# Kernel tuning notes

Measured on AMD Instinct MI355X. Metric: run time of the kernel, lower is better.

## Reference

```python
import jax, jax.numpy as jnp
import numpy as np

B, N, F_DIM, G_DIM, E_CAT, N_HEAD = 8, 1024, 128, 64, 2, 4
N_EDGES = 16384
L0 = 256          # NodeEmbedding hidden layer (layers=[256,128] -> last replaced by feature_size)
ALPHA = 0.5       # cfg.alpha
EPS = 1e-5        # BatchNorm eps
SLOPE = 0.01      # leaky_relu default negative slope


def _glorot(k, shape):
    stdv = float(np.sqrt(6.0 / (shape[-2] + shape[-1])))
    return jax.random.uniform(k, shape, jnp.float32, -stdv, stdv)


def setup_inputs() -> dict:
    key = jax.random.key(0)
    ks = jax.random.split(key, 8)
    X = jax.random.normal(ks[0], (B, N, F_DIM), dtype=jnp.float32)
    A = jax.random.randint(ks[1], (B, E_CAT, 2, N_EDGES), 0, N, dtype=jnp.int32)
    Ws = _glorot(ks[2], (E_CAT, N_HEAD * F_DIM, G_DIM))
    Wq = _glorot(ks[3], (E_CAT, N_HEAD * F_DIM, 1))
    Wv = _glorot(ks[4], (E_CAT, N_HEAD * F_DIM, 1))
    W_emb1 = _glorot(ks[5], (F_DIM, N_HEAD * E_CAT * G_DIM))   # Embedding1, bias=False
    W_lin0 = _glorot(ks[6], (L0, F_DIM))                        # NodeEmbedding linear0
    W_lin1 = _glorot(ks[7], (F_DIM, L0))                        # NodeEmbedding linear1
    return {"A": A, "X": X, "Ws": Ws, "Wq": Wq, "Wv": Wv,
            "W_emb1": W_emb1, "W_lin0": W_lin0, "W_lin1": W_lin1, "mini_batch": 1}


def _bn(x):
    # BatchNorm1d in training mode, affine = identity (weight=1, bias=0)
    mu = jnp.mean(x, axis=0)
    var = jnp.var(x, axis=0)  # biased variance, as torch uses for normalization
    return (x - mu) * jax.lax.rsqrt(var + EPS)


def _build_adj(A):
    # torch.sparse_coo_tensor(...).to_dense() sums duplicate edges
    adj = jnp.zeros((B, E_CAT, N, N), jnp.float32)
    b_idx = jnp.arange(B)[:, None, None]
    e_idx = jnp.arange(E_CAT)[None, :, None]
    return adj.at[b_idx, e_idx, A[:, :, 0], A[:, :, 1]].add(1.0)


def reference(A, X, Ws, Wq, Wv, W_emb1, W_lin0, W_lin1, mini_batch):
    Ws_r = Ws.reshape(E_CAT, N_HEAD, F_DIM, G_DIM)
    Wq_r = Wq.reshape(E_CAT, N_HEAD, F_DIM)   # last dim of Wq param is 1
    Wv_r = Wv.reshape(E_CAT, N_HEAD, F_DIM)

    Wh = jnp.einsum('bnf,ehfg->behng', X, Ws_r)   # [B,E,H,N,G]
    q = jnp.einsum('bnf,ehf->behn', X, Wq_r)      # [B,E,H,N]
    v = jnp.einsum('bnf,ehf->behn', X, Wv_r)

    adj = _build_adj(A)                            # [B,E,N,N]
    # e = (Wq @ Wv.T) * E, then leaky_relu and row softmax (dim=1 on [N,N] = last axis)
    scores = q[:, :, :, :, None] * v[:, :, :, None, :] * adj[:, :, None]
    scores = jnp.where(scores >= 0, scores, SLOPE * scores)
    a = jax.nn.softmax(scores, axis=-1)
    H = jnp.einsum('behnm,behmg->behng', a, Wh)    # [B,E,H,N,G]

    # concat over heads: [B,N, head-major (E*G)]
    H = H.transpose(0, 3, 2, 1, 4).reshape(B * N, N_HEAD * E_CAT * G_DIM)
    H = jax.nn.relu(H @ W_emb1.T)
    Xf = X.reshape(B * N, F_DIM)
    H = _bn((1.0 - ALPHA) * H + ALPHA * Xf)

    # NodeEmbedding: Linear -> BN -> ELU -> Linear
    Z = jax.nn.elu(_bn(H @ W_lin0.T))
    Z = Z @ W_lin1.T
    Z = _bn(H + Z)
    return Z.reshape(B, N, F_DIM)
```

## Files before the change

kernel.cpp:

```cpp
#include <hip/hip_runtime.h>
#include <hip/hip_bf16.h>

#define B_    8
#define N_    1024
#define F_    128
#define G_    64
#define EC    2
#define NHD   4
#define NE    16384
#define L0_   256
#define ALPHA_ 0.5f
#define EPS_   1e-5f
#define SLOPE_ 0.01f
#define ROWS  (B_*N_)
#define C1    (NHD*EC*G_)

typedef __attribute__((ext_vector_type(8))) short s8bf;
typedef __attribute__((ext_vector_type(4))) float f32x4;

__device__ __forceinline__ float ldv(const float* p, size_t i) { return p[i]; }
__device__ __forceinline__ float ldv(const __hip_bfloat16* p, size_t i) {
  unsigned short u = *(const unsigned short*)&p[i];
  return __uint_as_float((unsigned)u << 16);
}
__device__ __forceinline__ unsigned short f2b(float f) {
  unsigned u = __float_as_uint(f);
  u = (u + 0x7FFFu + ((u >> 16) & 1u)) >> 16;
  return (unsigned short)u;
}
__device__ __forceinline__ float b2f(unsigned short u) {
  return __uint_as_float((unsigned)u << 16);
}

__device__ __forceinline__ float wmaxf(float v) {
#pragma unroll
  for (int o = 32; o; o >>= 1) v = fmaxf(v, __shfl_xor(v, o, 64));
  return v;
}
__device__ __forceinline__ float wsumf(float v) {
#pragma unroll
  for (int o = 32; o; o >>= 1) v += __shfl_xor(v, o, 64);
  return v;
}

__global__ void k_prep(const unsigned short* Xu, int* flag,
                       const int* A, int* fill, int* colbuf) {
  int bid = blockIdx.x, tid = threadIdx.x;
  if (bid < 512) {
    int idx = bid * 256 + tid;
    unsigned short u = Xu[idx];
    if ((u & 0x7F80u) == 0x7F80u) atomicOr(flag, 1);
  } else {
    int idx = (bid - 512) * 256 + tid;
    int be = idx >> 14, i = idx & (NE - 1);
    int row = A[(size_t)(be * 2) * NE + i];
    int col = A[(size_t)(be * 2 + 1) * NE + i];
    int p = atomicAdd(&fill[be * N_ + row], 1);
    if (p < 64) colbuf[((size_t)(be * N_ + row)) * 64 + p] = col;
  }
}

__device__ __forceinline__ unsigned short cvt_at(const void* p, size_t i, int isf) {
  return isf ? f2b(((const float*)p)[i]) : ((const unsigned short*)p)[i];
}
template <typename T>
__device__ __forceinline__ void proj_qv16(const T* X, const T* Wq, const T* Wv,
                                          float* q, float* v, int pb) {
  int tid = threadIdx.x, lane = tid & 63, w = tid >> 6;
  int sub = lane >> 4, fl = lane & 15;
  int r = pb * 16 + w * 4 + sub;
  int n = r & (N_ - 1); int beh = r >> 10; int be = beh >> 2, h = beh & 3;
  int b = be >> 1, e = be & 1;
  const T* xr = X + (size_t)(b * N_ + n) * F_ + fl * 8;
  const T* wq = Wq + (e * NHD + h) * F_ + fl * 8;
  const T* wv = Wv + (e * NHD + h) * F_ + fl * 8;
  float dq = 0.f, dv = 0.f;
#pragma unroll
  for (int j = 0; j < 8; ++j) {
    float x = ldv(xr, j);
    dq += x * ldv(wq, j); dv += x * ldv(wv, j);
  }
#pragma unroll
  for (int o = 1; o < 16; o <<= 1) {
    dq += __shfl_xor(dq, o, 64); dv += __shfl_xor(dv, o, 64);
  }
  if (fl == 0) { q[r] = dq; v[r] = dv; }
}
__global__ void k_cvt2(const void* X, const void* Ws, const void* We1, const void* Wl1,
                       const void* Wl0, const void* Wq, const void* Wv,
                       unsigned short* Wsb, unsigned short* We1b,
                       unsigned short* Wl1b, unsigned short* Wl0b,
                       float* q, float* v, const int* flag) {
  int isf = *flag;
  int bid = blockIdx.x, t = threadIdx.x;
  if (bid < 256) {
    int i = bid * 256 + t; We1b[i] = cvt_at(We1, i, isf);
  } else if (bid < 384) {
    int i = (bid - 256) * 256 + t; Wl1b[i] = cvt_at(Wl1, i, isf);
  } else if (bid < 512) {
    int i = (bid - 384) * 256 + t; Wl0b[i] = cvt_at(Wl0, i, isf);
  } else if (bid < 768) {
    int i = (bid - 512) * 256 + t;
    int eh = i >> 13, rem = i & 8191;
    int g = rem >> 7, f = rem & 127;
    Wsb[eh * 8192 + g * 128 + f] = cvt_at(Ws, (size_t)eh * 8192 + f * 64 + g, isf);
  } else {
    int pb = bid - 768;
    if (isf) proj_qv16<float>((const float*)X, (const float*)Wq, (const float*)Wv, q, v, pb);
    else     proj_qv16<__hip_bfloat16>((const __hip_bfloat16*)X, (const __hip_bfloat16*)Wq,
                                       (const __hip_bfloat16*)Wv, q, v, pb);
  }
}

template <int K, int NC, int MODE, typename TA>
__device__ __forceinline__ void mfma_core_u(const TA* __restrict__ Araw,
                                            const float* sum, const float* ssq,
                                            const unsigned short* __restrict__ Wb,
                                            int r0, int c0, f32x4* acc) {
  int lane = threadIdx.x & 63; int q = lane >> 4, c15 = lane & 15;
  constexpr int RS = K / 8;
  const s8bf* bp = (const s8bf*)Wb + (size_t)(c0 + c15) * RS + q;
#pragma unroll
  for (int ks = 0; ks < K / 32; ++ks) {
    s8bf a;
    if constexpr (sizeof(TA) == 2) {
      const s8bf* ap = (const s8bf*)Araw + (size_t)(r0 + c15) * RS + q;
      a = ap[ks * 4];
    } else {
      const float* ap = (const float*)Araw + (size_t)(r0 + c15) * K + q * 8 + ks * 32;
      float av[8];
      *(float4*)&av[0] = *(const float4*)ap;
      *(float4*)&av[4] = *(const float4*)(ap + 4);
#pragma unroll
      for (int j = 0; j < 8; ++j) {
        float y = av[j];
        if (MODE) {
          int c = q * 8 + ks * 32 + j;
          float mean = sum[c] * (1.f / ROWS);
          float var = ssq[c] * (1.f / ROWS) - mean * mean;
          y = (y - mean) * rsqrtf(var + EPS_);
          if (MODE == 2) y = (y > 0.f) ? y : (expf(y) - 1.f);
        }
        a[j] = (short)f2b(y);
      }
    }
#pragma unroll
    for (int nc = 0; nc < NC; ++nc) {
      s8bf b = bp[(size_t)nc * 16 * RS + ks * 4];
      acc[nc] = __builtin_amdgcn_mfma_f32_16x16x32_bf16(a, b, acc[nc], 0, 0, 0);
    }
  }
}

__global__ __launch_bounds__(256) void k_whm(const void* X, const unsigned short* Wsb,
                                             unsigned short* Whb, float* S,
                                             const int* flag) {
  int w = threadIdx.x >> 6;
  int r0 = (blockIdx.x * 4 + w) * 16; int eh = blockIdx.y;
  f32x4 acc[4] = {{0,0,0,0},{0,0,0,0},{0,0,0,0},{0,0,0,0}};
  if (*flag)
    mfma_core_u<128, 4, 0, float>((const float*)X, nullptr, nullptr,
                                  Wsb + eh * 8192, r0, 0, acc);
  else
    mfma_core_u<128, 4, 0, unsigned short>((const unsigned short*)X, nullptr, nullptr,
                                           Wsb + eh * 8192, r0, 0, acc);
  int lane = threadIdx.x & 63, q = lane >> 4, c15 = lane & 15;
  int b = r0 >> 10; int beh = b * 8 + eh;
  unsigned short* WhB = Whb + ((size_t)beh * N_ + (r0 & (N_ - 1))) * G_;
#pragma unroll
  for (int nc = 0; nc < 4; ++nc) {
    float s = 0.f;
#pragma unroll
    for (int i = 0; i < 4; ++i) {
      float o = acc[nc][i];
      WhB[(size_t)(q * 4 + i) * G_ + nc * 16 + c15] = f2b(o);
      s += o;
    }
    s += __shfl_xor(s, 16, 64); s += __shfl_xor(s, 32, 64);
    if (lane < 16) atomicAdd(&S[(size_t)beh * G_ + nc * 16 + lane], s);
  }
}

__global__ __launch_bounds__(256) void k_attn3(const float* q, const float* v,
                                               const unsigned short* Whb,
                                               const float* S, const int* fill,
                                               const int* colbuf, unsigned short* Hcatb) {
  int tid = threadIdx.x, lane = tid & 63, w = tid >> 6;
  int xcd = blockIdx.x & 7, j = blockIdx.x >> 3;
  int be = (xcd << 1) | (j & 1);
  int n = (j >> 1) * 4 + w;
  int b = be >> 1, e = be & 1;
  int L = fill[be * N_ + n];
  int Lc = (L > 64) ? 64 : L;
  int myc = (lane < Lc) ? colbuf[((size_t)(be * N_ + n)) * 64 + lane] : -1;
  int cct = 0, firstk = 64;
  for (int k = 0; k < Lc; ++k) {
    int ck = __shfl(myc, k, 64);
    if (myc >= 0 && ck == myc) { cct++; if (k < firstk) firstk = k; }
  }
  bool act = (lane < Lc) && (firstk == lane);
  unsigned long long mask = __ballot(act);
  int pos = __popcll(mask & ((1ull << lane) - 1ull));
  __shared__ int s_col[4][64];
  __shared__ int s_cnt[4][64];
  s_col[w][lane] = 0; s_cnt[w][lane] = 0;
  if (act) { s_col[w][pos] = myc; s_cnt[w][pos] = cct; }
  int Ld = __popcll(mask);
  int colc = s_col[w][lane];
  int cntc = s_cnt[w][lane];
  int eg = lane >> 4, g4 = (lane & 15) << 2;
  size_t outb = ((size_t)(b * N_ + n)) * C1 + e * G_ + g4;
  float fN = (float)(N_ - Ld);
#pragma unroll
  for (int h = 0; h < 4; ++h) {
    int beh = (be << 2) | h;
    float qn = q[beh * N_ + n];
    float sc = -1e30f;
    if (lane < Ld) {
      float t = qn * v[beh * N_ + colc] * (float)cntc;
      sc = (t >= 0.f) ? t : SLOPE_ * t;
    }
    float M = fmaxf(0.f, wmaxf(sc));
    float Ej = (lane < Ld) ? expf(sc - M) : 0.f;
    float sumE = wsumf(Ej);
    float em = expf(-M);
    float Z = fN * em + sumE;
    float wgt = (lane < Ld) ? (Ej - em) / Z : 0.f;
    float4 accv = make_float4(0.f, 0.f, 0.f, 0.f);
    if (eg == 0) {
      float4 s4 = *(const float4*)&S[(size_t)beh * G_ + g4];
      float sca = em / Z;
      accv.x = sca * s4.x; accv.y = sca * s4.y; accv.z = sca * s4.z; accv.w = sca * s4.w;
    }
    const unsigned short* WhB = Whb + (size_t)beh * N_ * G_;
    for (int k0 = 0; k0 < Ld; k0 += 4) {
      int kk = k0 + eg;
      float wk = __shfl(wgt, kk, 64);
      int ck = __shfl(colc, kk, 64);
      ushort4 xu = *(const ushort4*)&WhB[(size_t)ck * G_ + g4];
      accv.x += wk * b2f(xu.x); accv.y += wk * b2f(xu.y);
      accv.z += wk * b2f(xu.z); accv.w += wk * b2f(xu.w);
    }
    accv.x += __shfl_xor(accv.x, 16, 64); accv.y += __shfl_xor(accv.y, 16, 64);
    accv.z += __shfl_xor(accv.z, 16, 64); accv.w += __shfl_xor(accv.w, 16, 64);
    accv.x += __shfl_xor(accv.x, 32, 64); accv.y += __shfl_xor(accv.y, 32, 64);
    accv.z += __shfl_xor(accv.z, 32, 64); accv.w += __shfl_xor(accv.w, 32, 64);
    if (lane < 16) {
      ushort4 o;
      o.x = f2b(accv.x); o.y = f2b(accv.y); o.z = f2b(accv.z); o.w = f2b(accv.w);
      *(ushort4*)&Hcatb[outb + (size_t)h * (EC * G_)] = o;
    }
  }
}

template <typename TX>
__device__ __forceinline__ void mm1_ep(f32x4* acc, const TX* X, float* T4,
                                       float* sum1, float* ssq1, int r0, int c0) {
  int lane = threadIdx.x & 63, q = lane >> 4, c15 = lane & 15;
#pragma unroll
  for (int nc = 0; nc < 2; ++nc) {
    int cc = c0 + nc * 16 + c15;
    float s = 0.f, s2 = 0.f;
#pragma unroll
    for (int i = 0; i < 4; ++i) {
      int rr = r0 + q * 4 + i;
      float o = fmaxf(acc[nc][i], 0.f);
      o = 0.5f * o + 0.5f * ldv(X, (size_t)rr * F_ + cc);
      T4[(size_t)rr * F_ + cc] = o;
      s += o; s2 += o * o;
    }
    s += __shfl_xor(s, 16, 64); s += __shfl_xor(s, 32, 64);
    s2 += __shfl_xor(s2, 16, 64); s2 += __shfl_xor(s2, 32, 64);
    if (lane < 16) {
      atomicAdd(&sum1[c0 + nc * 16 + lane], s);
      atomicAdd(&ssq1[c0 + nc * 16 + lane], s2);
    }
  }
}
__global__ __launch_bounds__(256) void k_mm1m(const unsigned short* Hcatb,
                                              const unsigned short* We1b, const void* X,
                                              float* T4, float* sum1, float* ssq1,
                                              const int* flag) {
  int w = threadIdx.x >> 6;
  int tile = blockIdx.x * 4 + w;
  int r0 = (tile >> 2) * 16, c0 = (tile & 3) * 32;
  f32x4 acc[2] = {{0,0,0,0},{0,0,0,0}};
  mfma_core_u<512, 2, 0, unsigned short>(Hcatb, nullptr, nullptr, We1b, r0, c0, acc);
  if (*flag) mm1_ep<float>(acc, (const float*)X, T4, sum1, ssq1, r0, c0);
  else       mm1_ep<__hip_bfloat16>(acc, (const __hip_bfloat16*)X, T4, sum1, ssq1, r0, c0);
}

__global__ __launch_bounds__(256) void k_lin0m(const float* T4, const float* sum1,
                                               const float* ssq1, const unsigned short* Wl0b,
                                               float* Z0, float* sum2, float* ssq2) {
  int w = threadIdx.x >> 6;
  int tile = blockIdx.x * 4 + w;
  int r0 = (tile >> 3) * 16, c0 = (tile & 7) * 32;
  f32x4 acc[2] = {{0,0,0,0},{0,0,0,0}};
  mfma_core_u<128, 2, 1, float>(T4, sum1, ssq1, Wl0b, r0, c0, acc);
  int lane = threadIdx.x & 63, q = lane >> 4, c15 = lane & 15;
#pragma unroll
  for (int nc = 0; nc < 2; ++nc) {
    int cc = c0 + nc * 16 + c15;
    float s = 0.f, s2 = 0.f;
#pragma unroll
    for (int i = 0; i < 4; ++i) {
      int rr = r0 + q * 4 + i;
      float o = acc[nc][i];
      Z0[(size_t)rr * L0_ + cc] = o;
      s += o; s2 += o * o;
    }
    s += __shfl_xor(s, 16, 64); s += __shfl_xor(s, 32, 64);
    s2 += __shfl_xor(s2, 16, 64); s2 += __shfl_xor(s2, 32, 64);
    if (lane < 16) {
      atomicAdd(&sum2[c0 + nc * 16 + lane], s);
      atomicAdd(&ssq2[c0 + nc * 16 + lane], s2);
    }
  }
}

__global__ __launch_bounds__(256) void k_lin1m(const float* Z0, const float* sum2,
                                               const float* ssq2, const unsigned short* Wl1b,
                                               const float* T4, const float* sum1,
                                               const float* ssq1,
                                               float* T6, float* sum3, float* ssq3) {
  int w = threadIdx.x >> 6;
  int tile = blockIdx.x * 4 + w;
  int r0 = (tile >> 2) * 16, c0 = (tile & 3) * 32;
  f32x4 acc[2] = {{0,0,0,0},{0,0,0,0}};
  mfma_core_u<256, 2, 2, float>(Z0, sum2, ssq2, Wl1b, r0, c0, acc);
  int lane = threadIdx.x & 63, q = lane >> 4, c15 = lane & 15;
#pragma unroll
  for (int nc = 0; nc < 2; ++nc) {
    int cc = c0 + nc * 16 + c15;
    float mean = sum1[cc] * (1.f / ROWS);
    float var = ssq1[cc] * (1.f / ROWS) - mean * mean;
    float rs = rsqrtf(var + EPS_);
    float s = 0.f, s2 = 0.f;
#pragma unroll
    for (int i = 0; i < 4; ++i) {
      int rr = r0 + q * 4 + i;
      float o = acc[nc][i] + (T4[(size_t)rr * F_ + cc] - mean) * rs;
      T6[(size_t)rr * F_ + cc] = o;
      s += o; s2 += o * o;
    }
    s += __shfl_xor(s, 16, 64); s += __shfl_xor(s, 32, 64);
    s2 += __shfl_xor(s2, 16, 64); s2 += __shfl_xor(s2, 32, 64);
    if (lane < 16) {
      atomicAdd(&sum3[c0 + nc * 16 + lane], s);
      atomicAdd(&ssq3[c0 + nc * 16 + lane], s2);
    }
  }
}

__global__ void k_norm_out(const float* in, void* out, const float* sum, const float* ssq,
                           const int* flag) {
  int idx = blockIdx.x * 256 + threadIdx.x; int c = idx & (F_ - 1);
  float mean = sum[c] * (1.f / ROWS);
  float var = ssq[c] * (1.f / ROWS) - mean * mean;
  float y = (in[idx] - mean) * rsqrtf(var + EPS_);
  if (*flag) ((float*)out)[idx] = y;
  else       ((__hip_bfloat16*)out)[idx] = __float2bfloat16(y);
}

extern "C" void kernel_launch(void* const* d_in, const int* in_sizes, int n_in,
                              void* d_out, int out_size, void* d_ws, size_t ws_size,
                              hipStream_t stream) {
  const int* A    = (const int*)d_in[0];
  const void* X   = d_in[1];
  const void* Ws  = d_in[2];
  const void* Wq  = d_in[3];
  const void* Wv  = d_in[4];
  const void* We1 = d_in[5];
  const void* Wl0 = d_in[6];
  const void* Wl1 = d_in[7];

  char* ws = (char*)d_ws;
  size_t off = 0;
  auto alloc = [&](size_t bytes) { size_t o = off; off += (bytes + 255) & ~(size_t)255; return o; };
  size_t o_fill   = alloc(16 * N_ * 4);
  size_t o_stats  = alloc(1024 * 4);
  size_t o_flag   = alloc(256);
  size_t o_S      = alloc((size_t)64 * G_ * 4);
  size_t zero_bytes = off;
  size_t o_colbuf = alloc((size_t)16 * N_ * 64 * 4);
  size_t o_q      = alloc((size_t)64 * N_ * 4);
  size_t o_v      = alloc((size_t)64 * N_ * 4);
  size_t o_Whb    = alloc((size_t)64 * N_ * G_ * 2);
  size_t o_Hcatb  = alloc((size_t)ROWS * C1 * 2);
  size_t o_T4     = alloc((size_t)ROWS * F_ * 4);
  size_t o_T6     = alloc((size_t)ROWS * F_ * 4);
  size_t o_Z0     = alloc((size_t)ROWS * L0_ * 4);
  size_t o_Wsb    = alloc((size_t)8 * G_ * F_ * 2);
  size_t o_We1b   = alloc((size_t)F_ * C1 * 2);
  size_t o_Wl1b   = alloc((size_t)F_ * L0_ * 2);
  size_t o_Wl0b   = alloc((size_t)L0_ * F_ * 2);

  int*   fill   = (int*)(ws + o_fill);
  float* stats  = (float*)(ws + o_stats);
  int*   flag   = (int*)(ws + o_flag);
  float* S      = (float*)(ws + o_S);
  int*   colbuf = (int*)(ws + o_colbuf);
  float* q      = (float*)(ws + o_q);
  float* v      = (float*)(ws + o_v);
  unsigned short* Whb   = (unsigned short*)(ws + o_Whb);
  unsigned short* Hcatb = (unsigned short*)(ws + o_Hcatb);
  float* T4     = (float*)(ws + o_T4);
  float* T6     = (float*)(ws + o_T6);
  float* Z0     = (float*)(ws + o_Z0);
  unsigned short* Wsb   = (unsigned short*)(ws + o_Wsb);
  unsigned short* We1b  = (unsigned short*)(ws + o_We1b);
  unsigned short* Wl1b  = (unsigned short*)(ws + o_Wl1b);
  unsigned short* Wl0b  = (unsigned short*)(ws + o_Wl0b);
  float* sum1 = stats,       *ssq1 = stats + 128;
  float* sum2 = stats + 256, *ssq2 = stats + 512;
  float* sum3 = stats + 768, *ssq3 = stats + 896;

  hipMemsetAsync(ws, 0, zero_bytes, stream);

  k_prep<<<1536, 256, 0, stream>>>((const unsigned short*)X, flag, A, fill, colbuf);
  k_cvt2<<<768 + 4096, 256, 0, stream>>>(X, Ws, We1, Wl1, Wl0, Wq, Wv,
                                         Wsb, We1b, Wl1b, Wl0b, q, v, flag);
  k_whm<<<dim3(ROWS / 64, 8), 256, 0, stream>>>(X, Wsb, Whb, S, flag);
  k_attn3<<<(16 * N_) / 4, 256, 0, stream>>>(q, v, Whb, S, fill, colbuf, Hcatb);
  k_mm1m<<<512, 256, 0, stream>>>(Hcatb, We1b, X, T4, sum1, ssq1, flag);
  k_lin0m<<<1024, 256, 0, stream>>>(T4, sum1, ssq1, Wl0b, Z0, sum2, ssq2);
  k_lin1m<<<512, 256, 0, stream>>>(Z0, sum2, ssq2, Wl1b, T4, sum1, ssq1,
                                   T6, sum3, ssq3);
  k_norm_out<<<(ROWS * F_) / 256, 256, 0, stream>>>(T6, d_out, sum3, ssq3, flag);

  (void)in_sizes; (void)n_in; (void)out_size; (void)ws_size;
}
```

Before: 212.5 us.

## Fuse all pipeline stages into one persistent kernel with grid barriers

Replaces the eight separate kernel launches with a single persistent kernel of 256 blocks. The stages are separated by atomic-counter grid barriers and each stage's work is redistributed over the fixed grid with strided loops. The aim is to remove launch overhead and inter-kernel gaps. In exchange, parallelism drops to 256 blocks of 256 threads (for example, attention now loops 16 rows per wave), and the spin barriers assume all blocks are co-resident.

```diff
diff --git a/kernel.cpp b/kernel.cpp
--- a/kernel.cpp
+++ b/kernel.cpp
@@ -31,7 +31,6 @@
 __device__ __forceinline__ float b2f(unsigned short u) {
   return __uint_as_float((unsigned)u << 16);
 }
-
 __device__ __forceinline__ float wmaxf(float v) {
 #pragma unroll
   for (int o = 32; o; o >>= 1) v = fmaxf(v, __shfl_xor(v, o, 64));
@@ -42,74 +41,19 @@
   for (int o = 32; o; o >>= 1) v += __shfl_xor(v, o, 64);
   return v;
 }
-
-__global__ void k_prep(const unsigned short* Xu, int* flag,
-                       const int* A, int* fill, int* colbuf) {
-  int bid = blockIdx.x, tid = threadIdx.x;
-  if (bid < 512) {
-    int idx = bid * 256 + tid;
-    unsigned short u = Xu[idx];
-    if ((u & 0x7F80u) == 0x7F80u) atomicOr(flag, 1);
-  } else {
-    int idx = (bid - 512) * 256 + tid;
-    int be = idx >> 14, i = idx & (NE - 1);
-    int row = A[(size_t)(be * 2) * NE + i];
-    int col = A[(size_t)(be * 2 + 1) * NE + i];
-    int p = atomicAdd(&fill[be * N_ + row], 1);
-    if (p < 64) colbuf[((size_t)(be * N_ + row)) * 64 + p] = col;
-  }
-}
-
 __device__ __forceinline__ unsigned short cvt_at(const void* p, size_t i, int isf) {
   return isf ? f2b(((const float*)p)[i]) : ((const unsigned short*)p)[i];
 }
-template <typename T>
-__device__ __forceinline__ void proj_qv16(const T* X, const T* Wq, const T* Wv,
-                                          float* q, float* v, int pb) {
-  int tid = threadIdx.x, lane = tid & 63, w = tid >> 6;
-  int sub = lane >> 4, fl = lane & 15;
-  int r = pb * 16 + w * 4 + sub;
-  int n = r & (N_ - 1); int beh = r >> 10; int be = beh >> 2, h = beh & 3;
-  int b = be >> 1, e = be & 1;
-  const T* xr = X + (size_t)(b * N_ + n) * F_ + fl * 8;
-  const T* wq = Wq + (e * NHD + h) * F_ + fl * 8;
-  const T* wv = Wv + (e * NHD + h) * F_ + fl * 8;
-  float dq = 0.f, dv = 0.f;
-#pragma unroll
-  for (int j = 0; j < 8; ++j) {
-    float x = ldv(xr, j);
-    dq += x * ldv(wq, j); dv += x * ldv(wv, j);
-  }
-#pragma unroll
-  for (int o = 1; o < 16; o <<= 1) {
-    dq += __shfl_xor(dq, o, 64); dv += __shfl_xor(dv, o, 64);
-  }
-  if (fl == 0) { q[r] = dq; v[r] = dv; }
-}
-__global__ void k_cvt2(const void* X, const void* Ws, const void* We1, const void* Wl1,
-                       const void* Wl0, const void* Wq, const void* Wv,
-                       unsigned short* Wsb, unsigned short* We1b,
-                       unsigned short* Wl1b, unsigned short* Wl0b,
-                       float* q, float* v, const int* flag) {
-  int isf = *flag;
-  int bid = blockIdx.x, t = threadIdx.x;
-  if (bid < 256) {
-    int i = bid * 256 + t; We1b[i] = cvt_at(We1, i, isf);
-  } else if (bid < 384) {
-    int i = (bid - 256) * 256 + t; Wl1b[i] = cvt_at(Wl1, i, isf);
-  } else if (bid < 512) {
-    int i = (bid - 384) * 256 + t; Wl0b[i] = cvt_at(Wl0, i, isf);
-  } else if (bid < 768) {
-    int i = (bid - 512) * 256 + t;
-    int eh = i >> 13, rem = i & 8191;
-    int g = rem >> 7, f = rem & 127;
-    Wsb[eh * 8192 + g * 128 + f] = cvt_at(Ws, (size_t)eh * 8192 + f * 64 + g, isf);
-  } else {
-    int pb = bid - 768;
-    if (isf) proj_qv16<float>((const float*)X, (const float*)Wq, (const float*)Wv, q, v, pb);
-    else     proj_qv16<__hip_bfloat16>((const __hip_bfloat16*)X, (const __hip_bfloat16*)Wq,
-                                       (const __hip_bfloat16*)Wv, q, v, pb);
-  }
+
+__device__ __forceinline__ void gbar(int* cnt) {
+  __syncthreads();
+  __threadfence();
+  if (threadIdx.x == 0) {
+    atomicAdd(cnt, 1);
+    while (atomicAdd(cnt, 0) < 256) __builtin_amdgcn_s_sleep(2);
+  }
+  __syncthreads();
+  __threadfence();
 }
 
 template <int K, int NC, int MODE, typename TA>
@@ -117,17 +61,17 @@
                                             const float* sum, const float* ssq,
                                             const unsigned short* __restrict__ Wb,
                                             int r0, int c0, f32x4* acc) {
-  int lane = threadIdx.x & 63; int q = lane >> 4, c15 = lane & 15;
+  int lane = threadIdx.x & 63; int qd = lane >> 4, c15 = lane & 15;
   constexpr int RS = K / 8;
-  const s8bf* bp = (const s8bf*)Wb + (size_t)(c0 + c15) * RS + q;
+  const s8bf* bp = (const s8bf*)Wb + (size_t)(c0 + c15) * RS + qd;
 #pragma unroll
   for (int ks = 0; ks < K / 32; ++ks) {
     s8bf a;
     if constexpr (sizeof(TA) == 2) {
-      const s8bf* ap = (const s8bf*)Araw + (size_t)(r0 + c15) * RS + q;
+      const s8bf* ap = (const s8bf*)Araw + (size_t)(r0 + c15) * RS + qd;
       a = ap[ks * 4];
     } else {
-      const float* ap = (const float*)Araw + (size_t)(r0 + c15) * K + q * 8 + ks * 32;
+      const float* ap = (const float*)Araw + (size_t)(r0 + c15) * K + qd * 8 + ks * 32;
       float av[8];
       *(float4*)&av[0] = *(const float4*)ap;
       *(float4*)&av[4] = *(const float4*)(ap + 4);
@@ -135,7 +79,7 @@
       for (int j = 0; j < 8; ++j) {
         float y = av[j];
         if (MODE) {
-          int c = q * 8 + ks * 32 + j;
+          int c = qd * 8 + ks * 32 + j;
           float mean = sum[c] * (1.f / ROWS);
           float var = ssq[c] * (1.f / ROWS) - mean * mean;
           y = (y - mean) * rsqrtf(var + EPS_);
@@ -152,215 +96,277 @@
   }
 }
 
-__global__ __launch_bounds__(256) void k_whm(const void* X, const unsigned short* Wsb,
-                                             unsigned short* Whb, float* S,
-                                             const int* flag) {
-  int w = threadIdx.x >> 6;
-  int r0 = (blockIdx.x * 4 + w) * 16; int eh = blockIdx.y;
-  f32x4 acc[4] = {{0,0,0,0},{0,0,0,0},{0,0,0,0},{0,0,0,0}};
-  if (*flag)
-    mfma_core_u<128, 4, 0, float>((const float*)X, nullptr, nullptr,
-                                  Wsb + eh * 8192, r0, 0, acc);
-  else
-    mfma_core_u<128, 4, 0, unsigned short>((const unsigned short*)X, nullptr, nullptr,
-                                           Wsb + eh * 8192, r0, 0, acc);
-  int lane = threadIdx.x & 63, q = lane >> 4, c15 = lane & 15;
-  int b = r0 >> 10; int beh = b * 8 + eh;
-  unsigned short* WhB = Whb + ((size_t)beh * N_ + (r0 & (N_ - 1))) * G_;
-#pragma unroll
-  for (int nc = 0; nc < 4; ++nc) {
-    float s = 0.f;
-#pragma unroll
-    for (int i = 0; i < 4; ++i) {
-      float o = acc[nc][i];
-      WhB[(size_t)(q * 4 + i) * G_ + nc * 16 + c15] = f2b(o);
-      s += o;
-    }
-    s += __shfl_xor(s, 16, 64); s += __shfl_xor(s, 32, 64);
-    if (lane < 16) atomicAdd(&S[(size_t)beh * G_ + nc * 16 + lane], s);
-  }
-}
-
-__global__ __launch_bounds__(256) void k_attn3(const float* q, const float* v,
-                                               const unsigned short* Whb,
-                                               const float* S, const int* fill,
-                                               const int* colbuf, unsigned short* Hcatb) {
-  int tid = threadIdx.x, lane = tid & 63, w = tid >> 6;
-  int xcd = blockIdx.x & 7, j = blockIdx.x >> 3;
-  int be = (xcd << 1) | (j & 1);
-  int n = (j >> 1) * 4 + w;
-  int b = be >> 1, e = be & 1;
-  int L = fill[be * N_ + n];
-  int Lc = (L > 64) ? 64 : L;
-  int myc = (lane < Lc) ? colbuf[((size_t)(be * N_ + n)) * 64 + lane] : -1;
-  int cct = 0, firstk = 64;
-  for (int k = 0; k < Lc; ++k) {
-    int ck = __shfl(myc, k, 64);
-    if (myc >= 0 && ck == myc) { cct++; if (k < firstk) firstk = k; }
-  }
-  bool act = (lane < Lc) && (firstk == lane);
-  unsigned long long mask = __ballot(act);
-  int pos = __popcll(mask & ((1ull << lane) - 1ull));
+__global__ __launch_bounds__(256) void k_mega(
+    const int* A, const void* X, const void* Ws, const void* Wq, const void* Wv,
+    const void* We1, const void* Wl0, const void* Wl1,
+    int* flag, int* fill, int* colbuf,
+    unsigned short* Wsb, unsigned short* We1b, unsigned short* Wl1b, unsigned short* Wl0b,
+    float* q, float* v, unsigned short* Whb, float* S, unsigned short* Hcatb,
+    float* T4, float* Z0, float* T6, float* stats, void* out, int* bars) {
   __shared__ int s_col[4][64];
   __shared__ int s_cnt[4][64];
-  s_col[w][lane] = 0; s_cnt[w][lane] = 0;
-  if (act) { s_col[w][pos] = myc; s_cnt[w][pos] = cct; }
-  int Ld = __popcll(mask);
-  int colc = s_col[w][lane];
-  int cntc = s_cnt[w][lane];
-  int eg = lane >> 4, g4 = (lane & 15) << 2;
-  size_t outb = ((size_t)(b * N_ + n)) * C1 + e * G_ + g4;
-  float fN = (float)(N_ - Ld);
-#pragma unroll
-  for (int h = 0; h < 4; ++h) {
-    int beh = (be << 2) | h;
-    float qn = q[beh * N_ + n];
-    float sc = -1e30f;
-    if (lane < Ld) {
-      float t = qn * v[beh * N_ + colc] * (float)cntc;
-      sc = (t >= 0.f) ? t : SLOPE_ * t;
-    }
-    float M = fmaxf(0.f, wmaxf(sc));
-    float Ej = (lane < Ld) ? expf(sc - M) : 0.f;
-    float sumE = wsumf(Ej);
-    float em = expf(-M);
-    float Z = fN * em + sumE;
-    float wgt = (lane < Ld) ? (Ej - em) / Z : 0.f;
-    float4 accv = make_float4(0.f, 0.f, 0.f, 0.f);
-    if (eg == 0) {
-      float4 s4 = *(const float4*)&S[(size_t)beh * G_ + g4];
-      float sca = em / Z;
-      accv.x = sca * s4.x; accv.y = sca * s4.y; accv.z = sca * s4.z; accv.w = sca * s4.w;
-    }
-    const unsigned short* WhB = Whb + (size_t)beh * N_ * G_;
-    for (int k0 = 0; k0 < Ld; k0 += 4) {
-      int kk = k0 + eg;
-      float wk = __shfl(wgt, kk, 64);
-      int ck = __shfl(colc, kk, 64);
-      ushort4 xu = *(const ushort4*)&WhB[(size_t)ck * G_ + g4];
-      accv.x += wk * b2f(xu.x); accv.y += wk * b2f(xu.y);
-      accv.z += wk * b2f(xu.z); accv.w += wk * b2f(xu.w);
-    }
-    accv.x += __shfl_xor(accv.x, 16, 64); accv.y += __shfl_xor(accv.y, 16, 64);
-    accv.z += __shfl_xor(accv.z, 16, 64); accv.w += __shfl_xor(accv.w, 16, 64);
-    accv.x += __shfl_xor(accv.x, 32, 64); accv.y += __shfl_xor(accv.y, 32, 64);
-    accv.z += __shfl_xor(accv.z, 32, 64); accv.w += __shfl_xor(accv.w, 32, 64);
-    if (lane < 16) {
+  int tid = threadIdx.x, lane = tid & 63, w = tid >> 6;
+  int gtid = blockIdx.x * 256 + tid;
+  int wid = blockIdx.x * 4 + w;
+  int qd = lane >> 4, c15 = lane & 15;
+  float* sum1 = stats,       *ssq1 = stats + 128;
+  float* sum2 = stats + 256, *ssq2 = stats + 512;
+  float* sum3 = stats + 768, *ssq3 = stats + 896;
+
+  {
+    const unsigned short* Xu = (const unsigned short*)X;
+    unsigned short u0 = Xu[gtid * 2], u1 = Xu[gtid * 2 + 1];
+    if (((u0 & 0x7F80u) == 0x7F80u) || ((u1 & 0x7F80u) == 0x7F80u)) atomicOr(flag, 1);
+#pragma unroll
+    for (int i = 0; i < 4; ++i) {
+      int idx = gtid + i * 65536;
+      int be = idx >> 14, ei = idx & (NE - 1);
+      int row = A[(size_t)(be * 2) * NE + ei];
+      int col = A[(size_t)(be * 2 + 1) * NE + ei];
+      int p = atomicAdd(&fill[be * N_ + row], 1);
+      if (p < 64) colbuf[((size_t)(be * N_ + row)) * 64 + p] = col;
+    }
+  }
+  gbar(bars + 0);
+  int isf = *flag;
+
+  {
+#pragma unroll
+    for (int i = 0; i < 3; ++i) {
+      int item = gtid + i * 65536;
+      if (item < 65536) { We1b[item] = cvt_at(We1, item, isf); }
+      else if (item < 98304) { int k = item - 65536; Wl1b[k] = cvt_at(Wl1, k, isf); }
+      else if (item < 131072) { int k = item - 98304; Wl0b[k] = cvt_at(Wl0, k, isf); }
+      else { int k = item - 131072; int eh = k >> 13, rem = k & 8191;
+             int g = rem >> 7, f = rem & 127;
+             Wsb[eh * 8192 + g * 128 + f] = cvt_at(Ws, (size_t)eh * 8192 + f * 64 + g, isf); }
+    }
+    int grp = gtid >> 4, fl = gtid & 15;
+    for (int j = 0; j < 16; ++j) {
+      int r = grp * 16 + j;
+      int n = r & (N_ - 1); int beh = r >> 10; int be = beh >> 2, h = beh & 3;
+      int b = be >> 1, e = be & 1;
+      float dq = 0.f, dv = 0.f;
+      if (isf) {
+        const float* xr = (const float*)X + (size_t)(b * N_ + n) * F_ + fl * 8;
+        const float* wq = (const float*)Wq + (e * NHD + h) * F_ + fl * 8;
+        const float* wv = (const float*)Wv + (e * NHD + h) * F_ + fl * 8;
+#pragma unroll
+        for (int t = 0; t < 8; ++t) { float x = xr[t]; dq += x * wq[t]; dv += x * wv[t]; }
+      } else {
+        const __hip_bfloat16* xr = (const __hip_bfloat16*)X + (size_t)(b * N_ + n) * F_ + fl * 8;
+        const __hip_bfloat16* wq = (const __hip_bfloat16*)Wq + (e * NHD + h) * F_ + fl * 8;
+        const __hip_bfloat16* wv = (const __hip_bfloat16*)Wv + (e * NHD + h) * F_ + fl * 8;
+#pragma unroll
+        for (int t = 0; t < 8; ++t) { float x = ldv(xr, t); dq += x * ldv(wq, t); dv += x * ldv(wv, t); }
+      }
+#pragma unroll
+      for (int o = 1; o < 16; o <<= 1) { dq += __shfl_xor(dq, o, 64); dv += __shfl_xor(dv, o, 64); }
+      if (fl == 0) { q[r] = dq; v[r] = dv; }
+    }
+  }
+  gbar(bars + 1);
+
+  for (int t = 0; t < 4; ++t) {
+    int tile = wid + t * 1024;
+    int eh = tile & 7, r0 = (tile >> 3) * 16;
+    f32x4 acc[4] = {{0,0,0,0},{0,0,0,0},{0,0,0,0},{0,0,0,0}};
+    if (isf) mfma_core_u<128, 4, 0, float>((const float*)X, nullptr, nullptr,
+                                           Wsb + eh * 8192, r0, 0, acc);
+    else     mfma_core_u<128, 4, 0, unsigned short>((const unsigned short*)X, nullptr, nullptr,
+                                                    Wsb + eh * 8192, r0, 0, acc);
+    int b = r0 >> 10; int beh = b * 8 + eh;
+    unsigned short* WhB = Whb + ((size_t)beh * N_ + (r0 & (N_ - 1))) * G_;
+#pragma unroll
+    for (int nc = 0; nc < 4; ++nc) {
+      float s = 0.f;
+#pragma unroll
+      for (int i = 0; i < 4; ++i) {
+        float o = acc[nc][i];
+        WhB[(size_t)(qd * 4 + i) * G_ + nc * 16 + c15] = f2b(o);
+        s += o;
+      }
+      s += __shfl_xor(s, 16, 64); s += __shfl_xor(s, 32, 64);
+      if (lane < 16) atomicAdd(&S[(size_t)beh * G_ + nc * 16 + lane], s);
+    }
+  }
+  gbar(bars + 2);
+
+  {
+    int x = blockIdx.x & 7, jj = blockIdx.x >> 3;
+    int be = (x << 1) | (jj >> 4);
+    int b = be >> 1, e = be & 1;
+    int nb = (jj & 15) * 64 + w * 16;
+    int eg = lane >> 4, g4 = (lane & 15) << 2;
+    for (int it = 0; it < 16; ++it) {
+      int n = nb + it;
+      int L = fill[be * N_ + n];
+      int Lc = (L > 64) ? 64 : L;
+      int myc = (lane < Lc) ? colbuf[((size_t)(be * N_ + n)) * 64 + lane] : -1;
+      int cct = 0, firstk = 64;
+      for (int k = 0; k < Lc; ++k) {
+        int ck = __shfl(myc, k, 64);
+        if (myc >= 0 && ck == myc) { cct++; if (k < firstk) firstk = k; }
+      }
+      bool act = (lane < Lc) && (firstk == lane);
+      unsigned long long mask = __ballot(act);
+      int pos = __popcll(mask & ((1ull << lane) - 1ull));
+      s_col[w][lane] = 0; s_cnt[w][lane] = 0;
+      if (act) { s_col[w][pos] = myc; s_cnt[w][pos] = cct; }
+      int Ld = __popcll(mask);
+      int colc = s_col[w][lane];
+      int cntc = s_cnt[w][lane];
+      size_t outb = ((size_t)(b * N_ + n)) * C1 + e * G_ + g4;
+      float fN = (float)(N_ - Ld);
+#pragma unroll
+      for (int h = 0; h < 4; ++h) {
+        int beh = (be << 2) | h;
+        float qn = q[beh * N_ + n];
+        float sc = -1e30f;
+        if (lane < Ld) {
+          float t = qn * v[beh * N_ + colc] * (float)cntc;
+          sc = (t >= 0.f) ? t : SLOPE_ * t;
+        }
+        float M = fmaxf(0.f, wmaxf(sc));
+        float Ej = (lane < Ld) ? expf(sc - M) : 0.f;
+        float sumE = wsumf(Ej);
+        float em = expf(-M);
+        float Z = fN * em + sumE;
+        float wgt = (lane < Ld) ? (Ej - em) / Z : 0.f;
+        float4 accv = make_float4(0.f, 0.f, 0.f, 0.f);
+        if (eg == 0) {
+          float4 s4 = *(const float4*)&S[(size_t)beh * G_ + g4];
+          float sca = em / Z;
+          accv.x = sca * s4.x; accv.y = sca * s4.y; accv.z = sca * s4.z; accv.w = sca * s4.w;
+        }
+        const unsigned short* WhB = Whb + (size_t)beh * N_ * G_;
+        for (int k0 = 0; k0 < Ld; k0 += 4) {
+          int kk = k0 + eg;
+          float wk = __shfl(wgt, kk, 64);
+          int ck = __shfl(colc, kk, 64);
+          ushort4 xu = *(const ushort4*)&WhB[(size_t)ck * G_ + g4];
+          accv.x += wk * b2f(xu.x); accv.y += wk * b2f(xu.y);
+          accv.z += wk * b2f(xu.z); accv.w += wk * b2f(xu.w);
+        }
+        accv.x += __shfl_xor(accv.x, 16, 64); accv.y += __shfl_xor(accv.y, 16, 64);
+        accv.z += __shfl_xor(accv.z, 16, 64); accv.w += __shfl_xor(accv.w, 16, 64);
+        accv.x += __shfl_xor(accv.x, 32, 64); accv.y += __shfl_xor(accv.y, 32, 64);
+        accv.z += __shfl_xor(accv.z, 32, 64); accv.w += __shfl_xor(accv.w, 32, 64);
+        if (lane < 16) {
+          ushort4 o;
+          o.x = f2b(accv.x); o.y = f2b(accv.y); o.z = f2b(accv.z); o.w = f2b(accv.w);
+          *(ushort4*)&Hcatb[outb + (size_t)h * (EC * G_)] = o;
+        }
+      }
+    }
+  }
+  gbar(bars + 3);
+
+  for (int t = 0; t < 2; ++t) {
+    int tile = wid + t * 1024;
+    int r0 = (tile >> 2) * 16, c0 = (tile & 3) * 32;
+    f32x4 acc[2] = {{0,0,0,0},{0,0,0,0}};
+    mfma_core_u<512, 2, 0, unsigned short>(Hcatb, nullptr, nullptr, We1b, r0, c0, acc);
+#pragma unroll
+    for (int nc = 0; nc < 2; ++nc) {
+      int cc = c0 + nc * 16 + c15;
+      float s = 0.f, s2 = 0.f;
+#pragma unroll
+      for (int i = 0; i < 4; ++i) {
+        int rr = r0 + qd * 4 + i;
+        float o = fmaxf(acc[nc][i], 0.f);
+        float xv = isf ? ldv((const float*)X, (size_t)rr * F_ + cc)
+                       : ldv((const __hip_bfloat16*)X, (size_t)rr * F_ + cc);
+        o = 0.5f * o + 0.5f * xv;
+        T4[(size_t)rr * F_ + cc] = o;
+        s += o; s2 += o * o;
+      }
+      s += __shfl_xor(s, 16, 64); s += __shfl_xor(s, 32, 64);
+      s2 += __shfl_xor(s2, 16, 64); s2 += __shfl_xor(s2, 32, 64);
+      if (lane < 16) {
+        atomicAdd(&sum1[c0 + nc * 16 + lane], s);
+        atomicAdd(&ssq1[c0 + nc * 16 + lane], s2);
+      }
+    }
+  }
+  gbar(bars + 4);
+
+  for (int t = 0; t < 4; ++t) {
+    int tile = wid + t * 1024;
+    int r0 = (tile >> 3) * 16, c0 = (tile & 7) * 32;
+    f32x4 acc[2] = {{0,0,0,0},{0,0,0,0}};
+    mfma_core_u<128, 2, 1, float>(T4, sum1, ssq1, Wl0b, r0, c0, acc);
+#pragma unroll
+    for (int nc = 0; nc < 2; ++nc) {
+      int cc = c0 + nc * 16 + c15;
+      float s = 0.f, s2 = 0.f;
+#pragma unroll
+      for (int i = 0; i < 4; ++i) {
+        int rr = r0 + qd * 4 + i;
+        float o = acc[nc][i];
+        Z0[(size_t)rr * L0_ + cc] = o;
+        s += o; s2 += o * o;
+      }
+      s += __shfl_xor(s, 16, 64); s += __shfl_xor(s, 32, 64);
+      s2 += __shfl_xor(s2, 16, 64); s2 += __shfl_xor(s2, 32, 64);
+      if (lane < 16) {
+        atomicAdd(&sum2[c0 + nc * 16 + lane], s);
+        atomicAdd(&ssq2[c0 + nc * 16 + lane], s2);
+      }
+    }
+  }
+  gbar(bars + 5);
+
+  for (int t = 0; t < 2; ++t) {
+    int tile = wid + t * 1024;
+    int r0 = (tile >> 2) * 16, c0 = (tile & 3) * 32;
+    f32x4 acc[2] = {{0,0,0,0},{0,0,0,0}};
+    mfma_core_u<256, 2, 2, float>(Z0, sum2, ssq2, Wl1b, r0, c0, acc);
+#pragma unroll
+    for (int nc = 0; nc < 2; ++nc) {
+      int cc = c0 + nc * 16 + c15;
+      float mean = sum1[cc] * (1.f / ROWS);
+      float var = ssq1[cc] * (1.f / ROWS) - mean * mean;
+      float rs = rsqrtf(var + EPS_);
+      float s = 0.f, s2 = 0.f;
+#pragma unroll
+      for (int i = 0; i < 4; ++i) {
+        int rr = r0 + qd * 4 + i;
+        float o = acc[nc][i] + (T4[(size_t)rr * F_ + cc] - mean) * rs;
+        T6[(size_t)rr * F_ + cc] = o;
+        s += o; s2 += o * o;
+      }
+      s += __shfl_xor(s, 16, 64); s += __shfl_xor(s, 32, 64);
+      s2 += __shfl_xor(s2, 16, 64); s2 += __shfl_xor(s2, 32, 64);
+      if (lane < 16) {
+        atomicAdd(&sum3[c0 + nc * 16 + lane], s);
+        atomicAdd(&ssq3[c0 + nc * 16 + lane], s2);
+      }
+    }
+  }
+  gbar(bars + 6);
+
+#pragma unroll
+  for (int i = 0; i < 4; ++i) {
+    int e0 = (i * 65536 + gtid) * 4;
+    float4 xv = *(const float4*)&T6[e0];
+    float y[4];
+    float* xp = &xv.x;
+#pragma unroll
+    for (int j = 0; j < 4; ++j) {
+      int c = (e0 + j) & (F_ - 1);
+      float mean = sum3[c] * (1.f / ROWS);
+      float var = ssq3[c] * (1.f / ROWS) - mean * mean;
+      y[j] = (xp[j] - mean) * rsqrtf(var + EPS_);
+    }
+    if (isf) {
+      *(float4*)&((float*)out)[e0] = make_float4(y[0], y[1], y[2], y[3]);
+    } else {
       ushort4 o;
-      o.x = f2b(accv.x); o.y = f2b(accv.y); o.z = f2b(accv.z); o.w = f2b(accv.w);
-      *(ushort4*)&Hcatb[outb + (size_t)h * (EC * G_)] = o;
-    }
-  }
-}
-
-template <typename TX>
-__device__ __forceinline__ void mm1_ep(f32x4* acc, const TX* X, float* T4,
-                                       float* sum1, float* ssq1, int r0, int c0) {
-  int lane = threadIdx.x & 63, q = lane >> 4, c15 = lane & 15;
-#pragma unroll
-  for (int nc = 0; nc < 2; ++nc) {
-    int cc = c0 + nc * 16 + c15;
-    float s = 0.f, s2 = 0.f;
-#pragma unroll
-    for (int i = 0; i < 4; ++i) {
-      int rr = r0 + q * 4 + i;
-      float o = fmaxf(acc[nc][i], 0.f);
-      o = 0.5f * o + 0.5f * ldv(X, (size_t)rr * F_ + cc);
-      T4[(size_t)rr * F_ + cc] = o;
-      s += o; s2 += o * o;
-    }
-    s += __shfl_xor(s, 16, 64); s += __shfl_xor(s, 32, 64);
-    s2 += __shfl_xor(s2, 16, 64); s2 += __shfl_xor(s2, 32, 64);
-    if (lane < 16) {
-      atomicAdd(&sum1[c0 + nc * 16 + lane], s);
-      atomicAdd(&ssq1[c0 + nc * 16 + lane], s2);
-    }
-  }
-}
-__global__ __launch_bounds__(256) void k_mm1m(const unsigned short* Hcatb,
-                                              const unsigned short* We1b, const void* X,
-                                              float* T4, float* sum1, float* ssq1,
-                                              const int* flag) {
-  int w = threadIdx.x >> 6;
-  int tile = blockIdx.x * 4 + w;
-  int r0 = (tile >> 2) * 16, c0 = (tile & 3) * 32;
-  f32x4 acc[2] = {{0,0,0,0},{0,0,0,0}};
-  mfma_core_u<512, 2, 0, unsigned short>(Hcatb, nullptr, nullptr, We1b, r0, c0, acc);
-  if (*flag) mm1_ep<float>(acc, (const float*)X, T4, sum1, ssq1, r0, c0);
-  else       mm1_ep<__hip_bfloat16>(acc, (const __hip_bfloat16*)X, T4, sum1, ssq1, r0, c0);
-}
-
-__global__ __launch_bounds__(256) void k_lin0m(const float* T4, const float* sum1,
-                                               const float* ssq1, const unsigned short* Wl0b,
-                                               float* Z0, float* sum2, float* ssq2) {
-  int w = threadIdx.x >> 6;
-  int tile = blockIdx.x * 4 + w;
-  int r0 = (tile >> 3) * 16, c0 = (tile & 7) * 32;
-  f32x4 acc[2] = {{0,0,0,0},{0,0,0,0}};
-  mfma_core_u<128, 2, 1, float>(T4, sum1, ssq1, Wl0b, r0, c0, acc);
-  int lane = threadIdx.x & 63, q = lane >> 4, c15 = lane & 15;
-#pragma unroll
-  for (int nc = 0; nc < 2; ++nc) {
-    int cc = c0 + nc * 16 + c15;
-    float s = 0.f, s2 = 0.f;
-#pragma unroll
-    for (int i = 0; i < 4; ++i) {
-      int rr = r0 + q * 4 + i;
-      float o = acc[nc][i];
-      Z0[(size_t)rr * L0_ + cc] = o;
-      s += o; s2 += o * o;
-    }
-    s += __shfl_xor(s, 16, 64); s += __shfl_xor(s, 32, 64);
-    s2 += __shfl_xor(s2, 16, 64); s2 += __shfl_xor(s2, 32, 64);
-    if (lane < 16) {
-      atomicAdd(&sum2[c0 + nc * 16 + lane], s);
-      atomicAdd(&ssq2[c0 + nc * 16 + lane], s2);
-    }
-  }
-}
-
-__global__ __launch_bounds__(256) void k_lin1m(const float* Z0, const float* sum2,
-                                               const float* ssq2, const unsigned short* Wl1b,
-                                               const float* T4, const float* sum1,
-                                               const float* ssq1,
-                                               float* T6, float* sum3, float* ssq3) {
-  int w = threadIdx.x >> 6;
-  int tile = blockIdx.x * 4 + w;
-  int r0 = (tile >> 2) * 16, c0 = (tile & 3) * 32;
-  f32x4 acc[2] = {{0,0,0,0},{0,0,0,0}};
-  mfma_core_u<256, 2, 2, float>(Z0, sum2, ssq2, Wl1b, r0, c0, acc);
-  int lane = threadIdx.x & 63, q = lane >> 4, c15 = lane & 15;
-#pragma unroll
-  for (int nc = 0; nc < 2; ++nc) {
-    int cc = c0 + nc * 16 + c15;
-    float mean = sum1[cc] * (1.f / ROWS);
-    float var = ssq1[cc] * (1.f / ROWS) - mean * mean;
-    float rs = rsqrtf(var + EPS_);
-    float s = 0.f, s2 = 0.f;
-#pragma unroll
-    for (int i = 0; i < 4; ++i) {
-      int rr = r0 + q * 4 + i;
-      float o = acc[nc][i] + (T4[(size_t)rr * F_ + cc] - mean) * rs;
-      T6[(size_t)rr * F_ + cc] = o;
-      s += o; s2 += o * o;
-    }
-    s += __shfl_xor(s, 16, 64); s += __shfl_xor(s, 32, 64);
-    s2 += __shfl_xor(s2, 16, 64); s2 += __shfl_xor(s2, 32, 64);
-    if (lane < 16) {
-      atomicAdd(&sum3[c0 + nc * 16 + lane], s);
-      atomicAdd(&ssq3[c0 + nc * 16 + lane], s2);
-    }
-  }
-}
-
-__global__ void k_norm_out(const float* in, void* out, const float* sum, const float* ssq,
-                           const int* flag) {
-  int idx = blockIdx.x * 256 + threadIdx.x; int c = idx & (F_ - 1);
-  float mean = sum[c] * (1.f / ROWS);
-  float var = ssq[c] * (1.f / ROWS) - mean * mean;
-  float y = (in[idx] - mean) * rsqrtf(var + EPS_);
-  if (*flag) ((float*)out)[idx] = y;
-  else       ((__hip_bfloat16*)out)[idx] = __float2bfloat16(y);
+      o.x = f2b(y[0]); o.y = f2b(y[1]); o.z = f2b(y[2]); o.w = f2b(y[3]);
+      *(ushort4*)&((__hip_bfloat16*)out)[e0] = o;
+    }
+  }
 }
 
 extern "C" void kernel_launch(void* const* d_in, const int* in_sizes, int n_in,
@@ -382,6 +388,7 @@
   size_t o_stats  = alloc(1024 * 4);
   size_t o_flag   = alloc(256);
   size_t o_S      = alloc((size_t)64 * G_ * 4);
+  size_t o_bars   = alloc(256);
   size_t zero_bytes = off;
   size_t o_colbuf = alloc((size_t)16 * N_ * 64 * 4);
   size_t o_q      = alloc((size_t)64 * N_ * 4);
@@ -400,6 +407,7 @@
   float* stats  = (float*)(ws + o_stats);
   int*   flag   = (int*)(ws + o_flag);
   float* S      = (float*)(ws + o_S);
+  int*   bars   = (int*)(ws + o_bars);
   int*   colbuf = (int*)(ws + o_colbuf);
   float* q      = (float*)(ws + o_q);
   float* v      = (float*)(ws + o_v);
@@ -412,22 +420,14 @@
   unsigned short* We1b  = (unsigned short*)(ws + o_We1b);
   unsigned short* Wl1b  = (unsigned short*)(ws + o_Wl1b);
   unsigned short* Wl0b  = (unsigned short*)(ws + o_Wl0b);
-  float* sum1 = stats,       *ssq1 = stats + 128;
-  float* sum2 = stats + 256, *ssq2 = stats + 512;
-  float* sum3 = stats + 768, *ssq3 = stats + 896;
 
   hipMemsetAsync(ws, 0, zero_bytes, stream);
 
-  k_prep<<<1536, 256, 0, stream>>>((const unsigned short*)X, flag, A, fill, colbuf);
-  k_cvt2<<<768 + 4096, 256, 0, stream>>>(X, Ws, We1, Wl1, Wl0, Wq, Wv,
-                                         Wsb, We1b, Wl1b, Wl0b, q, v, flag);
-  k_whm<<<dim3(ROWS / 64, 8), 256, 0, stream>>>(X, Wsb, Whb, S, flag);
-  k_attn3<<<(16 * N_) / 4, 256, 0, stream>>>(q, v, Whb, S, fill, colbuf, Hcatb);
-  k_mm1m<<<512, 256, 0, stream>>>(Hcatb, We1b, X, T4, sum1, ssq1, flag);
-  k_lin0m<<<1024, 256, 0, stream>>>(T4, sum1, ssq1, Wl0b, Z0, sum2, ssq2);
-  k_lin1m<<<512, 256, 0, stream>>>(Z0, sum2, ssq2, Wl1b, T4, sum1, ssq1,
-                                   T6, sum3, ssq3);
-  k_norm_out<<<(ROWS * F_) / 256, 256, 0, stream>>>(T6, d_out, sum3, ssq3, flag);
+  k_mega<<<256, 256, 0, stream>>>(A, X, Ws, Wq, Wv, We1, Wl0, Wl1,
+                                  flag, fill, colbuf,
+                                  Wsb, We1b, Wl1b, Wl0b,
+                                  q, v, Whb, S, Hcatb,
+                                  T4, Z0, T6, stats, d_out, bars);
 
   (void)in_sizes; (void)n_in; (void)out_size; (void)ws_size;
 }
```

Measured after the change: 659.4 us. 3.1x slower.
